# Optimization experiments

Hardware: AMD Instinct MI355X
Metric: run time of the kernel (lower is better)

Reference implementation:

```python
import jax, jax.numpy as jnp
import numpy as np

B, S, DIM = 2, 2048, 2048
N_HEADS, N_KV_HEADS = 16, 4
HEAD_DIM = DIM // N_HEADS  # 128
N_REP = N_HEADS // N_KV_HEADS  # 4


def setup_inputs() -> dict:
    key = jax.random.key(0)
    ks = jax.random.split(key, 7)
    x = jax.random.normal(ks[0], (B, S, DIM), dtype=jnp.float32)
    cos = jax.random.uniform(ks[1], (S, HEAD_DIM // 2), dtype=jnp.float32)
    sin = jax.random.uniform(ks[2], (S, HEAD_DIM // 2), dtype=jnp.float32)
    sc = 1.0 / np.sqrt(DIM)
    wq = jax.random.normal(ks[3], (DIM, N_HEADS * HEAD_DIM), dtype=jnp.float32) * sc
    wk = jax.random.normal(ks[4], (DIM, N_KV_HEADS * HEAD_DIM), dtype=jnp.float32) * sc
    wv = jax.random.normal(ks[5], (DIM, N_KV_HEADS * HEAD_DIM), dtype=jnp.float32) * sc
    wo = jax.random.normal(ks[6], (N_HEADS * HEAD_DIM, DIM), dtype=jnp.float32) * sc
    return {"x": x, "cos": cos, "sin": sin, "wq": wq, "wk": wk, "wv": wv, "wo": wo}


def _rope(t, cos, sin):
    # t: [B, S, H, hd]; cos/sin: [S, hd/2] -> broadcast as [1, S, 1, hd/2]
    tr, ti = t[..., ::2], t[..., 1::2]
    c = cos[None, :, None, :]
    s = sin[None, :, None, :]
    out_r = tr * c - ti * s
    out_i = tr * s + ti * c
    # interleave back: stack on new last axis then flatten
    return jnp.stack([out_r, out_i], axis=-1).reshape(t.shape)


def reference(x, cos, sin, wq, wk, wv, wo):
    bsz, seqlen, _ = x.shape
    xq = (x @ wq).reshape(bsz, seqlen, N_HEADS, HEAD_DIM)
    xk = (x @ wk).reshape(bsz, seqlen, N_KV_HEADS, HEAD_DIM)
    xv = (x @ wv).reshape(bsz, seqlen, N_KV_HEADS, HEAD_DIM)
    xq = _rope(xq, cos, sin)
    xk = _rope(xk, cos, sin)
    # GQA: repeat kv heads -> [B, S, H, hd]
    xk = jnp.repeat(xk, N_REP, axis=2)
    xv = jnp.repeat(xv, N_REP, axis=2)
    scale = 1.0 / jnp.sqrt(jnp.asarray(HEAD_DIM, dtype=x.dtype))
    scores = jnp.einsum("bqhd,bkhd->bhqk", xq, xk) * scale
    causal = jnp.tril(jnp.ones((seqlen, seqlen), dtype=bool))
    scores = jnp.where(causal[None, None, :, :], scores, jnp.asarray(-jnp.inf, dtype=scores.dtype))
    attn = jax.nn.softmax(scores, axis=-1)
    out = jnp.einsum("bhqk,bkhd->bqhd", attn, xv)
    out = out.reshape(bsz, seqlen, N_HEADS * HEAD_DIM)
    return out @ wo
```

## Files before the change

### kernel.cpp

```cpp
#include <hip/hip_runtime.h>
#include <stdint.h>

#define SEQ 2048

typedef uint16_t u16;
typedef uint32_t u32;
typedef __attribute__((ext_vector_type(4))) float f32x4;
typedef __attribute__((ext_vector_type(8))) __bf16 bf16x8;
typedef __attribute__((ext_vector_type(4))) __bf16 bf16x4;

__device__ __forceinline__ u16 f2bf(float f) {
    u32 u = __float_as_uint(f);
    u += 0x7FFFu + ((u >> 16) & 1u);
    return (u16)(u >> 16);
}
__device__ __forceinline__ float bf2f(u16 h) {
    return __uint_as_float(((u32)h) << 16);
}
__device__ __forceinline__ void async16(const void* g, void* l) {
    auto gp = (__attribute__((address_space(1))) void*)const_cast<void*>(g);
    auto lp = (__attribute__((address_space(3))) void*)l;
    __builtin_amdgcn_global_load_lds(gp, lp, 16, 0, 0);
}

__global__ __launch_bounds__(256) void convert_bf16(const float* __restrict__ src,
                                                    u16* __restrict__ dst) {
    int i = blockIdx.x * 256 + threadIdx.x;
    float4 v = ((const float4*)src)[i];
    u32 lo = (u32)f2bf(v.x) | ((u32)f2bf(v.y) << 16);
    u32 hi = (u32)f2bf(v.z) | ((u32)f2bf(v.w) << 16);
    ((uint2*)dst)[i] = make_uint2(lo, hi);
}

__global__ __launch_bounds__(256) void tconv(const float* __restrict__ src,
                                             u16* __restrict__ dst, int N, int K) {
    __shared__ float tile[64][65];
    const int n0 = blockIdx.x * 64, k0 = blockIdx.y * 64;
    const int tid = threadIdx.x;
#pragma unroll
    for (int p = 0; p < 4; p++) {
        int r = p * 16 + (tid >> 4);
        int c = (tid & 15) * 4;
        float4 v = *(const float4*)&src[(size_t)(k0 + r) * N + n0 + c];
        tile[r][c] = v.x; tile[r][c+1] = v.y; tile[r][c+2] = v.z; tile[r][c+3] = v.w;
    }
    __syncthreads();
#pragma unroll
    for (int p = 0; p < 4; p++) {
        int n = p * 16 + (tid >> 4);
        int kq = (tid & 15) * 4;
        u32 lo = (u32)f2bf(tile[kq+0][n]) | ((u32)f2bf(tile[kq+1][n]) << 16);
        u32 hi = (u32)f2bf(tile[kq+2][n]) | ((u32)f2bf(tile[kq+3][n]) << 16);
        *(uint2*)&dst[(size_t)(n0 + n) * K + k0 + kq] = make_uint2(lo, hi);
    }
}

template <bool F32OUT>
__global__ __launch_bounds__(256) void gemm128(const u16* __restrict__ A,
                                               const u16* __restrict__ Bt,
                                               void* __restrict__ Cv,
                                               int M, int N, int K) {
    __shared__ u16 lA[128 * 32];
    __shared__ u16 lB[128 * 32];
    const int tid = threadIdx.x;
    const int m0 = blockIdx.y * 128, n0 = blockIdx.x * 128;
    const int lane = tid & 63;
    const int lr = lane & 15, quad = lane >> 4;
    const int w = tid >> 6;
    const int wm = (w >> 1) * 64, wn = (w & 1) * 64;

    f32x4 acc[4][4] = {};

    const int srow = tid >> 2;
    const int schunk = (tid & 3) ^ (srow & 3);
    const u16* aS0 = A  + (size_t)(m0 + srow) * K + schunk * 8;
    const u16* aS1 = aS0 + (size_t)64 * K;
    const u16* bS0 = Bt + (size_t)(n0 + srow) * K + schunk * 8;
    const u16* bS1 = bS0 + (size_t)64 * K;
    u16* lAd = lA + tid * 8;
    u16* lBd = lB + tid * 8;

    for (int k0 = 0; k0 < K; k0 += 32) {
        __syncthreads();
        async16(aS0 + k0, lAd);
        async16(aS1 + k0, lAd + 2048);
        async16(bS0 + k0, lBd);
        async16(bS1 + k0, lBd + 2048);
        __syncthreads();
        bf16x8 af[4], bfr[4];
        const int cs = (quad ^ (lr & 3)) * 8;
#pragma unroll
        for (int i = 0; i < 4; i++)
            af[i] = *(const bf16x8*)&lA[(wm + i * 16 + lr) * 32 + cs];
#pragma unroll
        for (int i = 0; i < 4; i++)
            bfr[i] = *(const bf16x8*)&lB[(wn + i * 16 + lr) * 32 + cs];
#pragma unroll
        for (int mf = 0; mf < 4; mf++)
#pragma unroll
            for (int nf = 0; nf < 4; nf++)
                acc[mf][nf] = __builtin_amdgcn_mfma_f32_16x16x32_bf16(
                    af[mf], bfr[nf], acc[mf][nf], 0, 0, 0);
    }

#pragma unroll
    for (int mf = 0; mf < 4; mf++) {
#pragma unroll
        for (int nf = 0; nf < 4; nf++) {
#pragma unroll
            for (int r = 0; r < 4; r++) {
                size_t row = (size_t)(m0 + wm + mf * 16 + quad * 4 + r);
                size_t col = (size_t)(n0 + wn + nf * 16 + lr);
                if (F32OUT)
                    ((float*)Cv)[row * (size_t)N + col] = acc[mf][nf][r];
                else
                    ((u16*)Cv)[row * (size_t)N + col] = f2bf(acc[mf][nf][r]);
            }
        }
    }
}

__global__ __launch_bounds__(256) void rope_qk(u16* __restrict__ qkv,
                                               const float* __restrict__ cosp,
                                               const float* __restrict__ sinp) {
    const int t = blockIdx.x;
    const int spos = t & (SEQ - 1);
    const int tid = threadIdx.x;
    const float qscale = 0.088388347762f * 1.4426950408889634f;
    u16* row = qkv + (size_t)t * 3072;
#pragma unroll
    for (int it = 0; it < 5; it++) {
        int p = it * 256 + tid;
        int col, ci; float sc2;
        if (p < 1024) { col = 2 * p; ci = p & 63; sc2 = qscale; }
        else          { int p2 = p - 1024; col = 2048 + 2 * p2; ci = p2 & 63; sc2 = 1.0f; }
        u32 v = *(u32*)(row + col);
        float tr = bf2f((u16)(v & 0xFFFFu));
        float ti = bf2f((u16)(v >> 16));
        float cs = cosp[spos * 64 + ci];
        float sn = sinp[spos * 64 + ci];
        float orr = (tr * cs - ti * sn) * sc2;
        float oi  = (tr * sn + ti * cs) * sc2;
        *(u32*)(row + col) = (u32)f2bf(orr) | ((u32)f2bf(oi) << 16);
    }
}

__global__ __launch_bounds__(256) void transpose_v(const u16* __restrict__ qkv,
                                                   u16* __restrict__ vt) {
    __shared__ u16 tile[64][65];
    const int bid = blockIdx.x;
    const int dt = bid & 1;
    const int st = (bid >> 1) & 31;
    const int kh = (bid >> 6) & 3;
    const int b  = bid >> 8;
    const int tid = threadIdx.x;
#pragma unroll
    for (int pp = 0; pp < 2; pp++) {
        int r  = pp * 32 + (tid >> 3);
        int c8 = (tid & 7) * 8;
        const u16* src = qkv + (size_t)(b * SEQ + st * 64 + r) * 3072 + 2560 + kh * 128 + dt * 64 + c8;
        uint4 v = *(const uint4*)src;
        tile[r][c8+0] = (u16)(v.x & 0xFFFF); tile[r][c8+1] = (u16)(v.x >> 16);
        tile[r][c8+2] = (u16)(v.y & 0xFFFF); tile[r][c8+3] = (u16)(v.y >> 16);
        tile[r][c8+4] = (u16)(v.z & 0xFFFF); tile[r][c8+5] = (u16)(v.z >> 16);
        tile[r][c8+6] = (u16)(v.w & 0xFFFF); tile[r][c8+7] = (u16)(v.w >> 16);
    }
    __syncthreads();
#pragma unroll
    for (int pp = 0; pp < 2; pp++) {
        int dr = pp * 32 + (tid >> 3);
        int s8 = (tid & 7) * 8;
        uint4 o;
        o.x = (u32)tile[s8+0][dr] | ((u32)tile[s8+1][dr] << 16);
        o.y = (u32)tile[s8+2][dr] | ((u32)tile[s8+3][dr] << 16);
        o.z = (u32)tile[s8+4][dr] | ((u32)tile[s8+5][dr] << 16);
        o.w = (u32)tile[s8+6][dr] | ((u32)tile[s8+7][dr] << 16);
        u16* dst = vt + ((size_t)((b * 4 + kh) * 128 + dt * 64 + dr)) * SEQ + st * 64 + s8;
        *(uint4*)dst = o;
    }
}

__global__ __launch_bounds__(256, 2) void flash_attn(const u16* __restrict__ qkv,
                                                     const u16* __restrict__ vt,
                                                     u16* __restrict__ ob) {
    __shared__ u16 lK[2][64 * 128];
    __shared__ u16 lV[2][128 * 64];
    __shared__ u16 lP[4][32 * 64];
    const int bidx = blockIdx.x;
    int bh, qt;
    if (bidx < 256) { bh = bidx >> 3;         qt = 8 + (bidx & 7); }
    else            { bh = (bidx - 256) >> 3; qt = 7 - ((bidx - 256) & 7); }
    const int b = bh >> 4, h = bh & 15, kh = h >> 2;
    const int tid = threadIdx.x;
    const int w = tid >> 6, lane = tid & 63;
    const int lr = lane & 15, quad = lane >> 4;

    bf16x8 qf[2][4];
#pragma unroll
    for (int qi = 0; qi < 2; qi++) {
        const u16* qbase = qkv + (size_t)(b * SEQ + qt * 128 + w * 32 + qi * 16 + lr) * 3072 + h * 128;
#pragma unroll
        for (int kk = 0; kk < 4; kk++)
            qf[qi][kk] = *(const bf16x8*)(qbase + kk * 32 + quad * 8);
    }

    const int krow = tid >> 4;
    const int kchunk = (tid & 15) ^ krow;
    const int vrow = tid >> 3;
    const int vchunk = (tid & 7) ^ (vrow & 7);
    const u16* kRow = qkv + (size_t)b * SEQ * 3072 + 2048 + kh * 128
                    + (size_t)krow * 3072 + kchunk * 8;
    const u16* vRow = vt + (size_t)(b * 4 + kh) * 128 * SEQ
                    + (size_t)vrow * SEQ + vchunk * 8;

    f32x4 o[2][8] = {};
    float m_st[2] = {-1e30f, -1e30f};
    float l_st[2] = {0.f, 0.f};

    const int nkt = 2 * qt + 2;
    {
        u16* lKd = &lK[0][0] + tid * 8;
        u16* lVd = &lV[0][0] + tid * 8;
#pragma unroll
        for (int i = 0; i < 4; i++) async16(kRow + (size_t)(i * 16) * 3072, lKd + i * 2048);
#pragma unroll
        for (int i = 0; i < 4; i++) async16(vRow + (size_t)(i * 32) * SEQ, lVd + i * 2048);
    }
    const int qg = qt * 128 + w * 32 + lr;

    int nb = 0;
    for (int kt = 0; kt < nkt; kt++) {
        if (kt + 1 < nkt) {
            u16* lKd = &lK[nb ^ 1][0] + tid * 8;
            u16* lVd = &lV[nb ^ 1][0] + tid * 8;
#pragma unroll
            for (int i = 0; i < 4; i++)
                async16(kRow + (size_t)((kt + 1) * 64 + i * 16) * 3072, lKd + i * 2048);
#pragma unroll
            for (int i = 0; i < 4; i++)
                async16(vRow + (size_t)(i * 32) * SEQ + (kt + 1) * 64, lVd + i * 2048);
            asm volatile("s_waitcnt vmcnt(8)" ::: "memory");
        } else {
            asm volatile("s_waitcnt vmcnt(0)" ::: "memory");
        }
        asm volatile("s_barrier" ::: "memory");

        const u16* lKc = &lK[nb][0];
        const u16* lVc = &lV[nb][0];

        f32x4 sc[2][4] = {};
#pragma unroll
        for (int nf = 0; nf < 4; nf++) {
#pragma unroll
            for (int kk = 0; kk < 4; kk++) {
                bf16x8 ak = *(const bf16x8*)&lKc[(nf * 16 + lr) * 128 + (((kk * 4 + quad) ^ lr) * 8)];
                sc[0][nf] = __builtin_amdgcn_mfma_f32_16x16x32_bf16(ak, qf[0][kk], sc[0][nf], 0, 0, 0);
                sc[1][nf] = __builtin_amdgcn_mfma_f32_16x16x32_bf16(ak, qf[1][kk], sc[1][nf], 0, 0, 0);
            }
        }

        const bool diag = (kt >= 2 * qt);
        const int kb = kt * 64 + quad * 4;
#pragma unroll
        for (int qi = 0; qi < 2; qi++) {
            float ps[4][4];
            float mnew = m_st[qi];
            const int qrow_g = qg + qi * 16;
#pragma unroll
            for (int nf = 0; nf < 4; nf++)
#pragma unroll
                for (int r = 0; r < 4; r++) {
                    float v = sc[qi][nf][r];
                    if (diag && (kb + nf * 16 + r) > qrow_g) v = -1e30f;
                    ps[nf][r] = v;
                    mnew = fmaxf(mnew, v);
                }
            mnew = fmaxf(mnew, __shfl_xor(mnew, 16));
            mnew = fmaxf(mnew, __shfl_xor(mnew, 32));
            float rsum = 0.f;
#pragma unroll
            for (int nf = 0; nf < 4; nf++)
#pragma unroll
                for (int r = 0; r < 4; r++) {
                    float e = exp2f(ps[nf][r] - mnew);
                    ps[nf][r] = e;
                    rsum += e;
                }
            rsum += __shfl_xor(rsum, 16);
            rsum += __shfl_xor(rsum, 32);
            float alpha = exp2f(m_st[qi] - mnew);
            l_st[qi] = l_st[qi] * alpha + rsum;
            m_st[qi] = mnew;
#pragma unroll
            for (int r = 0; r < 4; r++) {
                float ar = __shfl(alpha, quad * 4 + r, 16);
#pragma unroll
                for (int nd = 0; nd < 8; nd++) o[qi][nd][r] *= ar;
            }
            const int qrow = qi * 16 + lr;
#pragma unroll
            for (int nf = 0; nf < 4; nf++) {
                u32 lo = (u32)f2bf(ps[nf][0]) | ((u32)f2bf(ps[nf][1]) << 16);
                u32 hi = (u32)f2bf(ps[nf][2]) | ((u32)f2bf(ps[nf][3]) << 16);
                int c = (nf * 4 + quad) ^ lr;
                *(uint2*)&lP[w][qrow * 64 + c * 4] = make_uint2(lo, hi);
            }
        }

#pragma unroll
        for (int kf = 0; kf < 2; kf++) {
            bf16x8 pa[2];
#pragma unroll
            for (int qi = 0; qi < 2; qi++) {
                int c0 = (kf * 8 + quad * 2) ^ lr;
                int c1 = (kf * 8 + quad * 2 + 1) ^ lr;
                bf16x4 p0 = *(const bf16x4*)&lP[w][(qi * 16 + lr) * 64 + c0 * 4];
                bf16x4 p1 = *(const bf16x4*)&lP[w][(qi * 16 + lr) * 64 + c1 * 4];
                pa[qi] = __builtin_shufflevector(p0, p1, 0, 1, 2, 3, 4, 5, 6, 7);
            }
#pragma unroll
            for (int nd = 0; nd < 8; nd++) {
                bf16x8 vb = *(const bf16x8*)&lVc[(nd * 16 + lr) * 64 + (((kf * 4 + quad) ^ (lr & 7)) * 8)];
                o[0][nd] = __builtin_amdgcn_mfma_f32_16x16x32_bf16(pa[0], vb, o[0][nd], 0, 0, 0);
                o[1][nd] = __builtin_amdgcn_mfma_f32_16x16x32_bf16(pa[1], vb, o[1][nd], 0, 0, 0);
            }
        }

        asm volatile("s_barrier" ::: "memory");
        nb ^= 1;
    }

#pragma unroll
    for (int qi = 0; qi < 2; qi++) {
        float rinv = 1.0f / l_st[qi];
        u16* obase = ob + (size_t)(b * SEQ + qt * 128 + w * 32 + qi * 16) * 2048 + h * 128;
#pragma unroll
        for (int r = 0; r < 4; r++) {
            float rv = __shfl(rinv, quad * 4 + r, 16);
#pragma unroll
            for (int nd = 0; nd < 8; nd++)
                obase[(quad * 4 + r) * 2048 + nd * 16 + lr] = f2bf(o[qi][nd][r] * rv);
        }
    }
}

extern "C" void kernel_launch(void* const* d_in, const int* in_sizes, int n_in,
                              void* d_out, int out_size, void* d_ws, size_t ws_size,
                              hipStream_t stream) {
    (void)in_sizes; (void)n_in; (void)out_size; (void)ws_size;
    const float* x    = (const float*)d_in[0];
    const float* cosp = (const float*)d_in[1];
    const float* sinp = (const float*)d_in[2];
    const float* wq   = (const float*)d_in[3];
    const float* wk   = (const float*)d_in[4];
    const float* wv   = (const float*)d_in[5];
    const float* wo   = (const float*)d_in[6];
    float* out = (float*)d_out;

    char* ws = (char*)d_ws;
    u16* xb    = (u16*)(ws);
    u16* qkvb  = (u16*)(ws + (size_t)16 * 1024 * 1024);
    u16* wqkvT = (u16*)(ws + (size_t)40 * 1024 * 1024);
    u16* woT   = (u16*)(ws + (size_t)52 * 1024 * 1024);
    u16* vtb   = (u16*)(ws + (size_t)60 * 1024 * 1024);
    u16* ob    = xb;

    convert_bf16<<<8192, 256, 0, stream>>>(x, xb);
    tconv<<<dim3(32, 32), 256, 0, stream>>>(wq, wqkvT, 2048, 2048);
    tconv<<<dim3( 8, 32), 256, 0, stream>>>(wk, wqkvT + (size_t)2048 * 2048, 512, 2048);
    tconv<<<dim3( 8, 32), 256, 0, stream>>>(wv, wqkvT + (size_t)2560 * 2048, 512, 2048);
    tconv<<<dim3(32, 32), 256, 0, stream>>>(wo, woT, 2048, 2048);
    gemm128<false><<<dim3(24, 32), 256, 0, stream>>>(xb, wqkvT, (void*)qkvb, 4096, 3072, 2048);
    rope_qk<<<4096, 256, 0, stream>>>(qkvb, cosp, sinp);
    transpose_v<<<512, 256, 0, stream>>>(qkvb, vtb);
    flash_attn<<<512, 256, 0, stream>>>(qkvb, vtb, ob);
    gemm128<true><<<dim3(16, 32), 256, 0, stream>>>(ob, woT, (void*)out, 4096, 2048, 2048);
}
```

Baseline: 351.6 us.

## Split KV range across two wave groups per block and fuse Q RoPE into attention

Flash attention now runs 512-thread blocks, each handling a balanced pair of query tiles sequentially. Two 4-wave groups split each tile's KV range and merge partial softmax states through shared memory. Q RoPE and scaling move into the attention Q load, so the separate rope kernel only rotates K. The KV loop loses its double buffering: each iteration waits for its own loads before computing, so memory latency is no longer overlapped. The causal mask is also applied on every tile rather than only diagonal ones.

```diff
diff --git a/kernel.cpp b/kernel.cpp
--- a/kernel.cpp
+++ b/kernel.cpp
@@ -120,29 +120,23 @@
     }
 }
 
-__global__ __launch_bounds__(256) void rope_qk(u16* __restrict__ qkv,
-                                               const float* __restrict__ cosp,
-                                               const float* __restrict__ sinp) {
+__global__ __launch_bounds__(256) void rope_k(u16* __restrict__ qkv,
+                                              const float* __restrict__ cosp,
+                                              const float* __restrict__ sinp) {
     const int t = blockIdx.x;
     const int spos = t & (SEQ - 1);
     const int tid = threadIdx.x;
-    const float qscale = 0.088388347762f * 1.4426950408889634f;
     u16* row = qkv + (size_t)t * 3072;
-#pragma unroll
-    for (int it = 0; it < 5; it++) {
-        int p = it * 256 + tid;
-        int col, ci; float sc2;
-        if (p < 1024) { col = 2 * p; ci = p & 63; sc2 = qscale; }
-        else          { int p2 = p - 1024; col = 2048 + 2 * p2; ci = p2 & 63; sc2 = 1.0f; }
-        u32 v = *(u32*)(row + col);
-        float tr = bf2f((u16)(v & 0xFFFFu));
-        float ti = bf2f((u16)(v >> 16));
-        float cs = cosp[spos * 64 + ci];
-        float sn = sinp[spos * 64 + ci];
-        float orr = (tr * cs - ti * sn) * sc2;
-        float oi  = (tr * sn + ti * cs) * sc2;
-        *(u32*)(row + col) = (u32)f2bf(orr) | ((u32)f2bf(oi) << 16);
-    }
+    const int col = 2048 + 2 * tid;
+    const int ci = tid & 63;
+    u32 v = *(u32*)(row + col);
+    float tr = bf2f((u16)(v & 0xFFFFu));
+    float ti = bf2f((u16)(v >> 16));
+    float cs = cosp[spos * 64 + ci];
+    float sn = sinp[spos * 64 + ci];
+    float orr = tr * cs - ti * sn;
+    float oi  = tr * sn + ti * cs;
+    *(u32*)(row + col) = (u32)f2bf(orr) | ((u32)f2bf(oi) << 16);
 }
 
 __global__ __launch_bounds__(256) void transpose_v(const u16* __restrict__ qkv,
@@ -180,167 +174,210 @@
     }
 }
 
-__global__ __launch_bounds__(256, 2) void flash_attn(const u16* __restrict__ qkv,
+__global__ __launch_bounds__(512, 2) void flash_attn(const u16* __restrict__ qkv,
                                                      const u16* __restrict__ vt,
+                                                     const float* __restrict__ cosp,
+                                                     const float* __restrict__ sinp,
                                                      u16* __restrict__ ob) {
-    __shared__ u16 lK[2][64 * 128];
-    __shared__ u16 lV[2][128 * 64];
-    __shared__ u16 lP[4][32 * 64];
+    __shared__ u16 sh[49152];
     const int bidx = blockIdx.x;
-    int bh, qt;
-    if (bidx < 256) { bh = bidx >> 3;         qt = 8 + (bidx & 7); }
-    else            { bh = (bidx - 256) >> 3; qt = 7 - ((bidx - 256) & 7); }
+    const int a  = bidx & 7;
+    const int bh = bidx >> 3;
     const int b = bh >> 4, h = bh & 15, kh = h >> 2;
     const int tid = threadIdx.x;
     const int w = tid >> 6, lane = tid & 63;
+    const int grp = w >> 2, wl = w & 3;
     const int lr = lane & 15, quad = lane >> 4;
-
-    bf16x8 qf[2][4];
-#pragma unroll
-    for (int qi = 0; qi < 2; qi++) {
-        const u16* qbase = qkv + (size_t)(b * SEQ + qt * 128 + w * 32 + qi * 16 + lr) * 3072 + h * 128;
-#pragma unroll
-        for (int kk = 0; kk < 4; kk++)
-            qf[qi][kk] = *(const bf16x8*)(qbase + kk * 32 + quad * 8);
-    }
-
-    const int krow = tid >> 4;
-    const int kchunk = (tid & 15) ^ krow;
-    const int vrow = tid >> 3;
-    const int vchunk = (tid & 7) ^ (vrow & 7);
+    const float qscale = 0.088388347762f * 1.4426950408889634f;
+
+    u16* lKg = sh + grp * 16384;
+    u16* lVg = lKg + 8192;
+    u16* lPw = sh + 32768 + w * 2048;
+
+    const int tidg = tid & 255;
+    const int krow = tidg >> 4;
+    const int kchunk = (tidg & 15) ^ krow;
+    const int vrow = tidg >> 3;
+    const int vchunk = (tidg & 7) ^ (vrow & 7);
     const u16* kRow = qkv + (size_t)b * SEQ * 3072 + 2048 + kh * 128
                     + (size_t)krow * 3072 + kchunk * 8;
     const u16* vRow = vt + (size_t)(b * 4 + kh) * 128 * SEQ
                     + (size_t)vrow * SEQ + vchunk * 8;
-
-    f32x4 o[2][8] = {};
-    float m_st[2] = {-1e30f, -1e30f};
-    float l_st[2] = {0.f, 0.f};
-
-    const int nkt = 2 * qt + 2;
-    {
-        u16* lKd = &lK[0][0] + tid * 8;
-        u16* lVd = &lV[0][0] + tid * 8;
-#pragma unroll
-        for (int i = 0; i < 4; i++) async16(kRow + (size_t)(i * 16) * 3072, lKd + i * 2048);
-#pragma unroll
-        for (int i = 0; i < 4; i++) async16(vRow + (size_t)(i * 32) * SEQ, lVd + i * 2048);
-    }
-    const int qg = qt * 128 + w * 32 + lr;
-
-    int nb = 0;
-    for (int kt = 0; kt < nkt; kt++) {
-        if (kt + 1 < nkt) {
-            u16* lKd = &lK[nb ^ 1][0] + tid * 8;
-            u16* lVd = &lV[nb ^ 1][0] + tid * 8;
+    u16* lKd = lKg + tidg * 8;
+    u16* lVd = lVg + tidg * 8;
+
+    float* mO = (float*)sh;
+    float* mM = (float*)(sh + 32768);
+
+    for (int p = 0; p < 2; p++) {
+        const int qt = p ? (7 - a) : (8 + a);
+        const int niters = p ? (8 - a) : (9 + a);
+        const int kt0 = grp * niters;
+
+        bf16x8 qf[2][4];
+#pragma unroll
+        for (int qi = 0; qi < 2; qi++) {
+            const int token = qt * 128 + wl * 32 + qi * 16 + lr;
+            const u16* qb = qkv + (size_t)(b * SEQ + token) * 3072 + h * 128;
+#pragma unroll
+            for (int kk = 0; kk < 4; kk++) {
+                uint4 raw = *(const uint4*)(qb + kk * 32 + quad * 8);
+                u32 rw[4] = {raw.x, raw.y, raw.z, raw.w};
+                union { u16 us[8]; bf16x8 v; } fr;
+#pragma unroll
+                for (int pp = 0; pp < 4; pp++) {
+                    int ci = kk * 16 + quad * 4 + pp;
+                    float cv = cosp[token * 64 + ci];
+                    float sv = sinp[token * 64 + ci];
+                    float tr = bf2f((u16)(rw[pp] & 0xFFFFu));
+                    float ti = bf2f((u16)(rw[pp] >> 16));
+                    fr.us[2 * pp]     = f2bf((tr * cv - ti * sv) * qscale);
+                    fr.us[2 * pp + 1] = f2bf((tr * sv + ti * cv) * qscale);
+                }
+                qf[qi][kk] = fr.v;
+            }
+        }
+
+        f32x4 o[2][8] = {};
+        float m_st[2] = {-1e30f, -1e30f};
+        float l_st[2] = {0.f, 0.f};
+        const int qg = qt * 128 + wl * 32 + lr;
+
+        for (int t = 0; t < niters; t++) {
+            const int kt = kt0 + t;
 #pragma unroll
             for (int i = 0; i < 4; i++)
-                async16(kRow + (size_t)((kt + 1) * 64 + i * 16) * 3072, lKd + i * 2048);
+                async16(kRow + (size_t)(kt * 64 + i * 16) * 3072, lKd + i * 2048);
 #pragma unroll
             for (int i = 0; i < 4; i++)
-                async16(vRow + (size_t)(i * 32) * SEQ + (kt + 1) * 64, lVd + i * 2048);
-            asm volatile("s_waitcnt vmcnt(8)" ::: "memory");
-        } else {
+                async16(vRow + (size_t)(i * 32) * SEQ + kt * 64, lVd + i * 2048);
             asm volatile("s_waitcnt vmcnt(0)" ::: "memory");
+            asm volatile("s_barrier" ::: "memory");
+
+            f32x4 sc[2][4] = {};
+#pragma unroll
+            for (int nf = 0; nf < 4; nf++) {
+#pragma unroll
+                for (int kk = 0; kk < 4; kk++) {
+                    bf16x8 ak = *(const bf16x8*)&lKg[(nf * 16 + lr) * 128 + (((kk * 4 + quad) ^ lr) * 8)];
+                    sc[0][nf] = __builtin_amdgcn_mfma_f32_16x16x32_bf16(ak, qf[0][kk], sc[0][nf], 0, 0, 0);
+                    sc[1][nf] = __builtin_amdgcn_mfma_f32_16x16x32_bf16(ak, qf[1][kk], sc[1][nf], 0, 0, 0);
+                }
+            }
+
+            const int kb = kt * 64 + quad * 4;
+#pragma unroll
+            for (int qi = 0; qi < 2; qi++) {
+                float ps[4][4];
+                float mnew = m_st[qi];
+                const int qrow_g = qg + qi * 16;
+#pragma unroll
+                for (int nf = 0; nf < 4; nf++)
+#pragma unroll
+                    for (int r = 0; r < 4; r++) {
+                        float v = sc[qi][nf][r];
+                        if ((kb + nf * 16 + r) > qrow_g) v = -1e30f;
+                        ps[nf][r] = v;
+                        mnew = fmaxf(mnew, v);
+                    }
+                mnew = fmaxf(mnew, __shfl_xor(mnew, 16));
+                mnew = fmaxf(mnew, __shfl_xor(mnew, 32));
+                float rsum = 0.f;
+#pragma unroll
+                for (int nf = 0; nf < 4; nf++)
+#pragma unroll
+                    for (int r = 0; r < 4; r++) {
+                        float e = exp2f(ps[nf][r] - mnew);
+                        ps[nf][r] = e;
+                        rsum += e;
+                    }
+                rsum += __shfl_xor(rsum, 16);
+                rsum += __shfl_xor(rsum, 32);
+                float alpha = exp2f(m_st[qi] - mnew);
+                l_st[qi] = l_st[qi] * alpha + rsum;
+                m_st[qi] = mnew;
+#pragma unroll
+                for (int r = 0; r < 4; r++) {
+                    float ar = __shfl(alpha, quad * 4 + r, 16);
+#pragma unroll
+                    for (int nd = 0; nd < 8; nd++) o[qi][nd][r] *= ar;
+                }
+                const int qrow = qi * 16 + lr;
+#pragma unroll
+                for (int nf = 0; nf < 4; nf++) {
+                    u32 lo = (u32)f2bf(ps[nf][0]) | ((u32)f2bf(ps[nf][1]) << 16);
+                    u32 hi = (u32)f2bf(ps[nf][2]) | ((u32)f2bf(ps[nf][3]) << 16);
+                    int c = (nf * 4 + quad) ^ lr;
+                    *(uint2*)&lPw[qrow * 64 + c * 4] = make_uint2(lo, hi);
+                }
+            }
+
+#pragma unroll
+            for (int kf = 0; kf < 2; kf++) {
+                bf16x8 pa[2];
+#pragma unroll
+                for (int qi = 0; qi < 2; qi++) {
+                    int c0 = (kf * 8 + quad * 2) ^ lr;
+                    int c1 = (kf * 8 + quad * 2 + 1) ^ lr;
+                    bf16x4 p0 = *(const bf16x4*)&lPw[(qi * 16 + lr) * 64 + c0 * 4];
+                    bf16x4 p1 = *(const bf16x4*)&lPw[(qi * 16 + lr) * 64 + c1 * 4];
+                    pa[qi] = __builtin_shufflevector(p0, p1, 0, 1, 2, 3, 4, 5, 6, 7);
+                }
+#pragma unroll
+                for (int nd = 0; nd < 8; nd++) {
+                    bf16x8 vb = *(const bf16x8*)&lVg[(nd * 16 + lr) * 64 + (((kf * 4 + quad) ^ (lr & 7)) * 8)];
+                    o[0][nd] = __builtin_amdgcn_mfma_f32_16x16x32_bf16(pa[0], vb, o[0][nd], 0, 0, 0);
+                    o[1][nd] = __builtin_amdgcn_mfma_f32_16x16x32_bf16(pa[1], vb, o[1][nd], 0, 0, 0);
+                }
+            }
+
+            asm volatile("s_barrier" ::: "memory");
         }
-        asm volatile("s_barrier" ::: "memory");
-
-        const u16* lKc = &lK[nb][0];
-        const u16* lVc = &lV[nb][0];
-
-        f32x4 sc[2][4] = {};
-#pragma unroll
-        for (int nf = 0; nf < 4; nf++) {
-#pragma unroll
-            for (int kk = 0; kk < 4; kk++) {
-                bf16x8 ak = *(const bf16x8*)&lKc[(nf * 16 + lr) * 128 + (((kk * 4 + quad) ^ lr) * 8)];
-                sc[0][nf] = __builtin_amdgcn_mfma_f32_16x16x32_bf16(ak, qf[0][kk], sc[0][nf], 0, 0, 0);
-                sc[1][nf] = __builtin_amdgcn_mfma_f32_16x16x32_bf16(ak, qf[1][kk], sc[1][nf], 0, 0, 0);
+
+        __syncthreads();
+        if (grp == 1) {
+#pragma unroll
+            for (int qi = 0; qi < 2; qi++) {
+#pragma unroll
+                for (int r = 0; r < 4; r++) {
+                    int row = wl * 32 + qi * 16 + quad * 4 + r;
+#pragma unroll
+                    for (int nd = 0; nd < 8; nd++)
+                        mO[row * 128 + nd * 16 + lr] = o[qi][nd][r];
+                }
+                if (quad == 0) {
+                    int rowl = wl * 32 + qi * 16 + lr;
+                    mM[rowl * 2]     = m_st[qi];
+                    mM[rowl * 2 + 1] = l_st[qi];
+                }
             }
         }
-
-        const bool diag = (kt >= 2 * qt);
-        const int kb = kt * 64 + quad * 4;
-#pragma unroll
-        for (int qi = 0; qi < 2; qi++) {
-            float ps[4][4];
-            float mnew = m_st[qi];
-            const int qrow_g = qg + qi * 16;
-#pragma unroll
-            for (int nf = 0; nf < 4; nf++)
+        __syncthreads();
+        if (grp == 0) {
+#pragma unroll
+            for (int qi = 0; qi < 2; qi++) {
+                int rowl = wl * 32 + qi * 16 + lr;
+                float m1 = mM[rowl * 2], l1 = mM[rowl * 2 + 1];
+                float M  = fmaxf(m_st[qi], m1);
+                float a0 = exp2f(m_st[qi] - M);
+                float a1 = exp2f(m1 - M);
+                float li = 1.0f / (l_st[qi] * a0 + l1 * a1);
+                u16* obase = ob + (size_t)(b * SEQ + qt * 128 + wl * 32 + qi * 16) * 2048 + h * 128;
 #pragma unroll
                 for (int r = 0; r < 4; r++) {
-                    float v = sc[qi][nf][r];
-                    if (diag && (kb + nf * 16 + r) > qrow_g) v = -1e30f;
-                    ps[nf][r] = v;
-                    mnew = fmaxf(mnew, v);
-                }
-            mnew = fmaxf(mnew, __shfl_xor(mnew, 16));
-            mnew = fmaxf(mnew, __shfl_xor(mnew, 32));
-            float rsum = 0.f;
-#pragma unroll
-            for (int nf = 0; nf < 4; nf++)
-#pragma unroll
-                for (int r = 0; r < 4; r++) {
-                    float e = exp2f(ps[nf][r] - mnew);
-                    ps[nf][r] = e;
-                    rsum += e;
-                }
-            rsum += __shfl_xor(rsum, 16);
-            rsum += __shfl_xor(rsum, 32);
-            float alpha = exp2f(m_st[qi] - mnew);
-            l_st[qi] = l_st[qi] * alpha + rsum;
-            m_st[qi] = mnew;
-#pragma unroll
-            for (int r = 0; r < 4; r++) {
-                float ar = __shfl(alpha, quad * 4 + r, 16);
-#pragma unroll
-                for (int nd = 0; nd < 8; nd++) o[qi][nd][r] *= ar;
-            }
-            const int qrow = qi * 16 + lr;
-#pragma unroll
-            for (int nf = 0; nf < 4; nf++) {
-                u32 lo = (u32)f2bf(ps[nf][0]) | ((u32)f2bf(ps[nf][1]) << 16);
-                u32 hi = (u32)f2bf(ps[nf][2]) | ((u32)f2bf(ps[nf][3]) << 16);
-                int c = (nf * 4 + quad) ^ lr;
-                *(uint2*)&lP[w][qrow * 64 + c * 4] = make_uint2(lo, hi);
+                    float a0b = __shfl(a0, quad * 4 + r, 16);
+                    float a1b = __shfl(a1, quad * 4 + r, 16);
+                    float lib = __shfl(li, quad * 4 + r, 16);
+                    int row = wl * 32 + qi * 16 + quad * 4 + r;
+#pragma unroll
+                    for (int nd = 0; nd < 8; nd++) {
+                        float val = (o[qi][nd][r] * a0b + mO[row * 128 + nd * 16 + lr] * a1b) * lib;
+                        obase[(quad * 4 + r) * 2048 + nd * 16 + lr] = f2bf(val);
+                    }
+                }
             }
         }
-
-#pragma unroll
-        for (int kf = 0; kf < 2; kf++) {
-            bf16x8 pa[2];
-#pragma unroll
-            for (int qi = 0; qi < 2; qi++) {
-                int c0 = (kf * 8 + quad * 2) ^ lr;
-                int c1 = (kf * 8 + quad * 2 + 1) ^ lr;
-                bf16x4 p0 = *(const bf16x4*)&lP[w][(qi * 16 + lr) * 64 + c0 * 4];
-                bf16x4 p1 = *(const bf16x4*)&lP[w][(qi * 16 + lr) * 64 + c1 * 4];
-                pa[qi] = __builtin_shufflevector(p0, p1, 0, 1, 2, 3, 4, 5, 6, 7);
-            }
-#pragma unroll
-            for (int nd = 0; nd < 8; nd++) {
-                bf16x8 vb = *(const bf16x8*)&lVc[(nd * 16 + lr) * 64 + (((kf * 4 + quad) ^ (lr & 7)) * 8)];
-                o[0][nd] = __builtin_amdgcn_mfma_f32_16x16x32_bf16(pa[0], vb, o[0][nd], 0, 0, 0);
-                o[1][nd] = __builtin_amdgcn_mfma_f32_16x16x32_bf16(pa[1], vb, o[1][nd], 0, 0, 0);
-            }
-        }
-
-        asm volatile("s_barrier" ::: "memory");
-        nb ^= 1;
-    }
-
-#pragma unroll
-    for (int qi = 0; qi < 2; qi++) {
-        float rinv = 1.0f / l_st[qi];
-        u16* obase = ob + (size_t)(b * SEQ + qt * 128 + w * 32 + qi * 16) * 2048 + h * 128;
-#pragma unroll
-        for (int r = 0; r < 4; r++) {
-            float rv = __shfl(rinv, quad * 4 + r, 16);
-#pragma unroll
-            for (int nd = 0; nd < 8; nd++)
-                obase[(quad * 4 + r) * 2048 + nd * 16 + lr] = f2bf(o[qi][nd][r] * rv);
-        }
+        __syncthreads();
     }
 }
 
@@ -371,8 +408,8 @@
     tconv<<<dim3( 8, 32), 256, 0, stream>>>(wv, wqkvT + (size_t)2560 * 2048, 512, 2048);
     tconv<<<dim3(32, 32), 256, 0, stream>>>(wo, woT, 2048, 2048);
     gemm128<false><<<dim3(24, 32), 256, 0, stream>>>(xb, wqkvT, (void*)qkvb, 4096, 3072, 2048);
-    rope_qk<<<4096, 256, 0, stream>>>(qkvb, cosp, sinp);
+    rope_k<<<4096, 256, 0, stream>>>(qkvb, cosp, sinp);
     transpose_v<<<512, 256, 0, stream>>>(qkvb, vtb);
-    flash_attn<<<512, 256, 0, stream>>>(qkvb, vtb, ob);
+    flash_attn<<<256, 512, 0, stream>>>(qkvb, vtb, cosp, sinp, ob);
     gemm128<true><<<dim3(16, 32), 256, 0, stream>>>(ob, woT, (void*)out, 4096, 2048, 2048);
 }
```

After: 339.5 us. 3.4% less time.
